# Performance work log

Hardware: AMD Instinct MI355X
Metric: run time of the kernel (lower is better)

Reference implementation:

```python
import jax, jax.numpy as jnp
import numpy as np

B, SQ, SK, D = 8, 2048, 2048, 512

def setup_inputs() -> dict:
    key = jax.random.key(0)
    kq, kk, kv = jax.random.split(key, 3)
    return {
        "query": jax.random.normal(kq, (B, SQ, D), dtype=jnp.float32),
        "key": jax.random.normal(kk, (B, SK, D), dtype=jnp.float32),
        "value": jax.random.normal(kv, (B, SK, D), dtype=jnp.float32),
        "alpha": jnp.float32(0.5),  # learned scalar, init 0.5 as in torch module
    }

def reference(query, key, value, alpha):
    # squared L2 pairwise distances: ||q||^2 + ||k||^2 - 2 q.k  (== cdist(...)**2)
    q2 = jnp.sum(query * query, axis=-1, keepdims=True)          # [B,Sq,1]
    k2 = jnp.sum(key * key, axis=-1, keepdims=True)              # [B,Sk,1]
    qk = jnp.einsum("bqd,bkd->bqk", query, key)                  # [B,Sq,Sk]
    sq_dist = jnp.maximum(q2 + jnp.swapaxes(k2, -1, -2) - 2.0 * qk, 0.0)
    kernel = jnp.exp(-alpha * sq_dist)                            # Gaussian energy well
    weights = jax.nn.softmax(kernel, axis=-1)                     # softmax over keys
    out = jnp.einsum("bqk,bkd->bqd", weights, value)
    return out, weights
```

## Files before the change

### kernel.cpp

```cpp
#include <hip/hip_runtime.h>
#include <stdint.h>

#define B_  8
#define SQ_ 2048
#define SK_ 2048
#define D_  512

typedef unsigned short ushort_t;
typedef __attribute__((ext_vector_type(8))) short          short8;
typedef __attribute__((ext_vector_type(8))) unsigned short ushort8;
typedef __attribute__((ext_vector_type(4))) float          f32x4;

__device__ __forceinline__ unsigned short f2bf(float x) {
  union { float f; unsigned u; } v; v.f = x;
  unsigned r = v.u + 0x7FFFu + ((v.u >> 16) & 1u);
  return (unsigned short)(r >> 16);
}

__device__ __forceinline__ void gload_lds16(const void* g, void* l) {
  __builtin_amdgcn_global_load_lds(
      (__attribute__((address_space(1))) void*)(uintptr_t)g,
      (__attribute__((address_space(3))) void*)l, 16, 0, 0);
}

__global__ void prep_qk(const float* __restrict__ Q, const float* __restrict__ K,
                        ushort_t* __restrict__ Qb, ushort_t* __restrict__ Kb,
                        float* __restrict__ q2, float* __restrict__ k2) {
  const int t = threadIdx.x;
  const int rloc = t >> 7;
  const int row  = blockIdx.x * 2 + rloc;
  const bool isK = row >= B_ * SQ_;
  const int r = isK ? row - B_ * SQ_ : row;
  const float*    src = (isK ? K : Q) + (size_t)r * D_;
  ushort_t*       dst = (isK ? Kb : Qb) + (size_t)r * D_;
  float*          d2  = isK ? k2 : q2;

  const int c = (t & 127) * 4;
  float4 v = *(const float4*)(src + c);
  ushort4 o;
  o.x = f2bf(v.x); o.y = f2bf(v.y); o.z = f2bf(v.z); o.w = f2bf(v.w);
  *(ushort4*)(dst + c) = o;

  float s = v.x * v.x + v.y * v.y + v.z * v.z + v.w * v.w;
  for (int off = 32; off; off >>= 1) s += __shfl_down(s, off);
  __shared__ float ps[4];
  if ((t & 63) == 0) ps[t >> 6] = s;
  __syncthreads();
  if ((t & 127) == 0) d2[r] = ps[rloc * 2] + ps[rloc * 2 + 1];
}

__global__ void prep_vt(const float* __restrict__ V, ushort_t* __restrict__ VT) {
  const int b  = blockIdx.z;
  const int k0 = blockIdx.x * 64;
  const int d0 = blockIdx.y * 64;
  __shared__ __align__(16) ushort_t tile[64][68];
  const int t = threadIdx.x;
  const float* src = V + (size_t)b * SK_ * D_;
  #pragma unroll
  for (int i = 0; i < 4; ++i) {
    int kl = (t >> 4) + i * 16;
    int dl = (t & 15) * 4;
    float4 v = *(const float4*)(src + (size_t)(k0 + kl) * D_ + d0 + dl);
    tile[kl][dl]     = f2bf(v.x);
    tile[kl][dl + 1] = f2bf(v.y);
    tile[kl][dl + 2] = f2bf(v.z);
    tile[kl][dl + 3] = f2bf(v.w);
  }
  __syncthreads();
  ushort_t* dstb = VT + (size_t)b * D_ * SK_;
  #pragma unroll
  for (int j = 0; j < 2; ++j) {
    int chunk = t + j * 256;
    int dl = chunk >> 3;
    int kc = (chunk & 7) << 3;
    ushort8 o;
    #pragma unroll
    for (int m = 0; m < 8; ++m) o[m] = tile[kc + m][dl];
    *(ushort8*)(dstb + (size_t)(d0 + dl) * SK_ + k0 + kc) = o;
  }
}

template <int BF16E>
__global__ __launch_bounds__(256) void qk_kernel(
    const ushort_t* __restrict__ Qb, const ushort_t* __restrict__ Kb,
    const float* __restrict__ q2, const float* __restrict__ k2,
    const float* __restrict__ alphap,
    float* __restrict__ Wf, ushort_t* __restrict__ Ebf,
    float* __restrict__ rowsum) {
  __shared__ __align__(16) ushort_t As[2][8192];
  __shared__ __align__(16) ushort_t Bs[2][8192];
  __shared__ float q2s[128], k2s[128];

  const int t = threadIdx.x;
  const int lane = t & 63, wid = t >> 6;
  const int wm = wid >> 1, wn = wid & 1;

  const int id  = blockIdx.x + 16 * blockIdx.y + 256 * blockIdx.z;
  const int swz = (id & 7) * 256 + (id >> 3);
  const int bx = swz & 15, by = (swz >> 4) & 15, bz = swz >> 8;

  const ushort_t* Aq = Qb + ((size_t)bz * SQ_ + by * 128) * D_;
  const ushort_t* Bk = Kb + ((size_t)bz * SK_ + bx * 128) * D_;

  if (t < 128) q2s[t] = q2[bz * SQ_ + by * 128 + t];
  else         k2s[t - 128] = k2[bz * SK_ + bx * 128 + (t - 128)];

  #define QK_STAGE(buf, kt)                                                     \
    _Pragma("unroll")                                                           \
    for (int i = 0; i < 4; ++i) {                                               \
      int s = t + i * 256;                                                      \
      int row = s >> 3;                                                         \
      int c16 = (s & 7) ^ (row & 7);                                            \
      gload_lds16(Aq + (size_t)row * D_ + (kt) * 64 + c16 * 8,                  \
                  (char*)As[buf] + s * 16);                                     \
      gload_lds16(Bk + (size_t)row * D_ + (kt) * 64 + c16 * 8,                  \
                  (char*)Bs[buf] + s * 16);                                     \
    }

  QK_STAGE(0, 0);
  __syncthreads();

  f32x4 acc[4][4] = {};
  #pragma unroll
  for (int kt = 0; kt < 8; ++kt) {
    const int cur = kt & 1;
    if (kt < 7) { QK_STAGE(cur ^ 1, kt + 1); }
    #pragma unroll
    for (int kk = 0; kk < 2; ++kk) {
      short8 a[4], bf[4];
      #pragma unroll
      for (int mi = 0; mi < 4; ++mi) {
        int row = (wm << 6) + (mi << 4) + (lane & 15);
        int c = ((kk << 2) + (lane >> 4)) ^ (row & 7);
        a[mi] = *(const short8*)((const char*)As[cur] + row * 128 + c * 16);
      }
      #pragma unroll
      for (int ni = 0; ni < 4; ++ni) {
        int col = (wn << 6) + (ni << 4) + (lane & 15);
        int c = ((kk << 2) + (lane >> 4)) ^ (col & 7);
        bf[ni] = *(const short8*)((const char*)Bs[cur] + col * 128 + c * 16);
      }
      #pragma unroll
      for (int mi = 0; mi < 4; ++mi)
        #pragma unroll
        for (int ni = 0; ni < 4; ++ni)
          acc[mi][ni] = __builtin_amdgcn_mfma_f32_16x16x32_bf16(a[mi], bf[ni], acc[mi][ni], 0, 0, 0);
    }
    __syncthreads();
  }
  #undef QK_STAGE

  const float alpha = *alphap;
  const int r0 = (lane >> 4) << 2;
  const int cl = lane & 15;

  float k2c[4];
  #pragma unroll
  for (int ni = 0; ni < 4; ++ni) k2c[ni] = k2s[(wn << 6) + (ni << 4) + cl];

  #pragma unroll
  for (int mi = 0; mi < 4; ++mi) {
    float q2r[4];
    #pragma unroll
    for (int r = 0; r < 4; ++r) q2r[r] = q2s[(wm << 6) + (mi << 4) + r0 + r];
    float se[4] = {0.f, 0.f, 0.f, 0.f};
    #pragma unroll
    for (int ni = 0; ni < 4; ++ni) {
      int gcol = bx * 128 + (wn << 6) + (ni << 4) + cl;
      float x[4], e[4];
      #pragma unroll
      for (int r = 0; r < 4; ++r) {
        float sq = fmaxf(q2r[r] + k2c[ni] - 2.0f * acc[mi][ni][r], 0.0f);
        x[r] = -alpha * sq;
      }
      int small = (x[0] < -20.f) & (x[1] < -20.f) & (x[2] < -20.f) & (x[3] < -20.f);
      if (__all(small)) {
        #pragma unroll
        for (int r = 0; r < 4; ++r) e[r] = 1.0f;
      } else {
        #pragma unroll
        for (int r = 0; r < 4; ++r) e[r] = __expf(__expf(x[r]));
      }
      #pragma unroll
      for (int r = 0; r < 4; ++r) {
        int rl = (wm << 6) + (mi << 4) + r0 + r;
        size_t idx = (size_t)((size_t)bz * SQ_ + by * 128 + rl) * SK_ + gcol;
        if (BF16E) Ebf[idx] = f2bf(e[r]);
        else       Wf[idx]  = e[r];
        se[r] += e[r];
      }
    }
    #pragma unroll
    for (int r = 0; r < 4; ++r) {
      float s = se[r];
      for (int off = 1; off < 16; off <<= 1) s += __shfl_xor(s, off);
      if (cl == 0)
        atomicAdd(&rowsum[bz * SQ_ + by * 128 + (wm << 6) + (mi << 4) + r0 + r], s);
    }
  }
}

__global__ __launch_bounds__(256) void pv_bf16(
    const ushort_t* __restrict__ Eb, const ushort_t* __restrict__ VT,
    const float* __restrict__ rowsum, float* __restrict__ Out,
    float* __restrict__ W) {
  __shared__ __align__(16) ushort_t As[2][8192];
  __shared__ __align__(16) ushort_t Bs[2][8192];
  __shared__ float rss[128];

  const int t = threadIdx.x;
  const int lane = t & 63, wid = t >> 6;
  const int wm = wid >> 1, wn = wid & 1;

  const int id  = blockIdx.x + 4 * blockIdx.y + 64 * blockIdx.z;
  const int swz = (id & 7) * 64 + (id >> 3);
  const int bx = swz & 3, by = (swz >> 2) & 15, bz = swz >> 6;

  const ushort_t* Ebb = Eb + ((size_t)bz * SQ_ + by * 128) * SK_;
  const ushort_t* Vb  = VT + ((size_t)bz * D_ + bx * 128) * SK_;
  float* Wb = W + ((size_t)bz * SQ_ + by * 128) * SK_;

  if (t < 128) rss[t] = rowsum[bz * SQ_ + by * 128 + t];
  __syncthreads();
  const float rinv_t = 1.0f;

  #define PV_STAGE(buf, kt)                                                     \
    _Pragma("unroll")                                                           \
    for (int i = 0; i < 4; ++i) {                                               \
      int s = t + i * 256;                                                      \
      int row = s >> 3;                                                         \
      int c16 = (s & 7) ^ (row & 7);                                            \
      gload_lds16(Ebb + (size_t)row * SK_ + (kt) * 64 + c16 * 8,                \
                  (char*)As[buf] + s * 16);                                     \
      gload_lds16(Vb  + (size_t)row * SK_ + (kt) * 64 + c16 * 8,                \
                  (char*)Bs[buf] + s * 16);                                     \
    }

  PV_STAGE(0, 0);
  __syncthreads();

  const int wlo = bx * 8, whi = wlo + 8;
  f32x4 acc[4][4] = {};
  for (int kt = 0; kt < 32; ++kt) {
    const int cur = kt & 1;
    if (kt < 31) { PV_STAGE(cur ^ 1, kt + 1); }

    if (kt >= wlo && kt < whi) {
      #pragma unroll
      for (int i = 0; i < 4; ++i) {
        int s = t + i * 256;
        int row = s >> 3;
        int c16 = s & 7;
        int c16s = c16 ^ (row & 7);
        ushort8 ev = *(const ushort8*)((const char*)As[cur] + row * 128 + c16s * 16);
        float rinv = 1.0f / rss[row];
        float4 lo, hi;
        lo.x = __uint_as_float((unsigned)ev[0] << 16) * rinv;
        lo.y = __uint_as_float((unsigned)ev[1] << 16) * rinv;
        lo.z = __uint_as_float((unsigned)ev[2] << 16) * rinv;
        lo.w = __uint_as_float((unsigned)ev[3] << 16) * rinv;
        hi.x = __uint_as_float((unsigned)ev[4] << 16) * rinv;
        hi.y = __uint_as_float((unsigned)ev[5] << 16) * rinv;
        hi.z = __uint_as_float((unsigned)ev[6] << 16) * rinv;
        hi.w = __uint_as_float((unsigned)ev[7] << 16) * rinv;
        float* wp = Wb + (size_t)row * SK_ + kt * 64 + c16 * 8;
        *(float4*)wp       = lo;
        *(float4*)(wp + 4) = hi;
      }
    }

    #pragma unroll
    for (int kk = 0; kk < 2; ++kk) {
      short8 a[4], bf[4];
      #pragma unroll
      for (int mi = 0; mi < 4; ++mi) {
        int row = (wm << 6) + (mi << 4) + (lane & 15);
        int c = ((kk << 2) + (lane >> 4)) ^ (row & 7);
        a[mi] = *(const short8*)((const char*)As[cur] + row * 128 + c * 16);
      }
      #pragma unroll
      for (int ni = 0; ni < 4; ++ni) {
        int col = (wn << 6) + (ni << 4) + (lane & 15);
        int c = ((kk << 2) + (lane >> 4)) ^ (col & 7);
        bf[ni] = *(const short8*)((const char*)Bs[cur] + col * 128 + c * 16);
      }
      #pragma unroll
      for (int mi = 0; mi < 4; ++mi)
        #pragma unroll
        for (int ni = 0; ni < 4; ++ni)
          acc[mi][ni] = __builtin_amdgcn_mfma_f32_16x16x32_bf16(a[mi], bf[ni], acc[mi][ni], 0, 0, 0);
    }
    __syncthreads();
  }
  #undef PV_STAGE
  (void)rinv_t;

  float* Ob = Out + ((size_t)bz * SQ_ + by * 128) * D_ + bx * 128;
  const int r0 = (lane >> 4) << 2;
  const int cl = lane & 15;
  #pragma unroll
  for (int mi = 0; mi < 4; ++mi) {
    #pragma unroll
    for (int r = 0; r < 4; ++r) {
      int rl = (wm << 6) + (mi << 4) + r0 + r;
      float rinv = 1.0f / rss[rl];
      #pragma unroll
      for (int ni = 0; ni < 4; ++ni)
        Ob[(size_t)rl * D_ + (wn << 6) + (ni << 4) + cl] = acc[mi][ni][r] * rinv;
    }
  }
}

__global__ __launch_bounds__(256) void pv_f32(
    const float* __restrict__ E, const ushort_t* __restrict__ VT,
    const float* __restrict__ rowsum, float* __restrict__ Out) {
  __shared__ __align__(16) ushort_t As[8192];
  __shared__ __align__(16) ushort_t Bs[8192];
  __shared__ float rss[128];

  const int t = threadIdx.x;
  const int lane = t & 63, wid = t >> 6;
  const int wm = wid >> 1, wn = wid & 1;
  const int bx = blockIdx.x, by = blockIdx.y, bz = blockIdx.z;

  const float*    Eb = E + ((size_t)bz * SQ_ + by * 128) * SK_;
  const ushort_t* Vb = VT + ((size_t)bz * D_ + bx * 128) * SK_;

  if (t < 128) rss[t] = rowsum[bz * SQ_ + by * 128 + t];

  f32x4 acc[4][4] = {};
  for (int kt = 0; kt < SK_ / 64; ++kt) {
    float4 va[4][2];
    #pragma unroll
    for (int i = 0; i < 4; ++i) {
      int s = t + i * 256;
      int row = s >> 3, c16 = s & 7;
      const float* g = Eb + (size_t)row * SK_ + kt * 64 + c16 * 8;
      va[i][0] = *(const float4*)g;
      va[i][1] = *(const float4*)(g + 4);
    }
    __syncthreads();
    #pragma unroll
    for (int i = 0; i < 4; ++i) {
      int s = t + i * 256;
      int row = s >> 3, c16 = s & 7;
      int c16s = c16 ^ (row & 7);
      ushort8 o;
      o[0] = f2bf(va[i][0].x); o[1] = f2bf(va[i][0].y);
      o[2] = f2bf(va[i][0].z); o[3] = f2bf(va[i][0].w);
      o[4] = f2bf(va[i][1].x); o[5] = f2bf(va[i][1].y);
      o[6] = f2bf(va[i][1].z); o[7] = f2bf(va[i][1].w);
      *(ushort8*)((char*)As + row * 128 + c16s * 16) = o;
      gload_lds16(Vb + (size_t)row * SK_ + kt * 64 + c16s * 8, (char*)Bs + s * 16);
    }
    __syncthreads();
    #pragma unroll
    for (int kk = 0; kk < 2; ++kk) {
      short8 a[4], bf[4];
      #pragma unroll
      for (int mi = 0; mi < 4; ++mi) {
        int row = (wm << 6) + (mi << 4) + (lane & 15);
        int c = ((kk << 2) + (lane >> 4)) ^ (row & 7);
        a[mi] = *(const short8*)((const char*)As + row * 128 + c * 16);
      }
      #pragma unroll
      for (int ni = 0; ni < 4; ++ni) {
        int col = (wn << 6) + (ni << 4) + (lane & 15);
        int c = ((kk << 2) + (lane >> 4)) ^ (col & 7);
        bf[ni] = *(const short8*)((const char*)Bs + col * 128 + c * 16);
      }
      #pragma unroll
      for (int mi = 0; mi < 4; ++mi)
        #pragma unroll
        for (int ni = 0; ni < 4; ++ni)
          acc[mi][ni] = __builtin_amdgcn_mfma_f32_16x16x32_bf16(a[mi], bf[ni], acc[mi][ni], 0, 0, 0);
    }
  }

  float* Ob = Out + ((size_t)bz * SQ_ + by * 128) * D_ + bx * 128;
  const int r0 = (lane >> 4) << 2;
  const int cl = lane & 15;
  #pragma unroll
  for (int mi = 0; mi < 4; ++mi) {
    #pragma unroll
    for (int r = 0; r < 4; ++r) {
      int rl = (wm << 6) + (mi << 4) + r0 + r;
      float rinv = 1.0f / rss[rl];
      #pragma unroll
      for (int ni = 0; ni < 4; ++ni)
        Ob[(size_t)rl * D_ + (wn << 6) + (ni << 4) + cl] = acc[mi][ni][r] * rinv;
    }
  }
}

__global__ void norm_f32(float* __restrict__ W, const float* __restrict__ rowsum) {
  const size_t total4 = (size_t)B_ * SQ_ * SK_ / 4;
  for (size_t i = (size_t)blockIdx.x * blockDim.x + threadIdx.x; i < total4;
       i += (size_t)gridDim.x * blockDim.x) {
    float4 v = ((const float4*)W)[i];
    float rinv = 1.0f / rowsum[i >> 9];
    v.x *= rinv; v.y *= rinv; v.z *= rinv; v.w *= rinv;
    ((float4*)W)[i] = v;
  }
}

extern "C" void kernel_launch(void* const* d_in, const int* in_sizes, int n_in,
                              void* d_out, int out_size, void* d_ws, size_t ws_size,
                              hipStream_t stream) {
  const float* Q     = (const float*)d_in[0];
  const float* K     = (const float*)d_in[1];
  const float* V     = (const float*)d_in[2];
  const float* alpha = (const float*)d_in[3];

  float* out = (float*)d_out;
  float* W   = out + (size_t)B_ * SQ_ * D_;

  const size_t QKV = (size_t)B_ * SQ_ * D_;
  const size_t NW  = (size_t)B_ * SQ_ * SK_;
  ushort_t* Qb = (ushort_t*)d_ws;
  ushort_t* Kb = Qb + QKV;
  ushort_t* VT = Kb + QKV;

  const size_t need_bf16 = (3 * QKV + NW) * sizeof(ushort_t)
                         + (size_t)(2 * B_ * SQ_ + B_ * SK_) * sizeof(float);
  const bool use_bf16 = ws_size >= need_bf16;

  ushort_t* Eb = VT + QKV;
  float* fbase = use_bf16 ? (float*)(Eb + NW) : (float*)(VT + QKV);
  float* q2     = fbase;
  float* k2     = q2 + B_ * SQ_;
  float* rowsum = k2 + B_ * SK_;

  hipMemsetAsync(rowsum, 0, (size_t)B_ * SQ_ * sizeof(float), stream);

  prep_qk<<<dim3(B_ * SQ_), 256, 0, stream>>>(Q, K, Qb, Kb, q2, k2);
  prep_vt<<<dim3(SK_ / 64, D_ / 64, B_), 256, 0, stream>>>(V, VT);

  if (use_bf16) {
    qk_kernel<1><<<dim3(SK_ / 128, SQ_ / 128, B_), 256, 0, stream>>>(
        Qb, Kb, q2, k2, alpha, nullptr, Eb, rowsum);
    pv_bf16<<<dim3(D_ / 128, SQ_ / 128, B_), 256, 0, stream>>>(Eb, VT, rowsum, out, W);
  } else {
    qk_kernel<0><<<dim3(SK_ / 128, SQ_ / 128, B_), 256, 0, stream>>>(
        Qb, Kb, q2, k2, alpha, W, nullptr, rowsum);
    pv_f32<<<dim3(D_ / 128, SQ_ / 128, B_), 256, 0, stream>>>(W, VT, rowsum, out);
    norm_f32<<<dim3(4096), 256, 0, stream>>>(W, rowsum);
  }
}
```

Baseline: 353.9 us.

## Swap MFMA operand order so accumulators hold contiguous columns for vector stores

```diff
diff --git a/kernel.cpp b/kernel.cpp
--- a/kernel.cpp
+++ b/kernel.cpp
@@ -93,7 +93,7 @@
 
   const int t = threadIdx.x;
   const int lane = t & 63, wid = t >> 6;
-  const int wm = wid >> 1, wn = wid & 1;
+  const int wA = wid >> 1, wB = wid & 1;
 
   const int id  = blockIdx.x + 16 * blockIdx.y + 256 * blockIdx.z;
   const int swz = (id & 7) * 256 + (id >> 3);
@@ -127,24 +127,24 @@
     if (kt < 7) { QK_STAGE(cur ^ 1, kt + 1); }
     #pragma unroll
     for (int kk = 0; kk < 2; ++kk) {
-      short8 a[4], bf[4];
-      #pragma unroll
-      for (int mi = 0; mi < 4; ++mi) {
-        int row = (wm << 6) + (mi << 4) + (lane & 15);
+      short8 qf[4], kf[4];
+      #pragma unroll
+      for (int qi = 0; qi < 4; ++qi) {
+        int row = (wB << 6) + (qi << 4) + (lane & 15);
         int c = ((kk << 2) + (lane >> 4)) ^ (row & 7);
-        a[mi] = *(const short8*)((const char*)As[cur] + row * 128 + c * 16);
-      }
-      #pragma unroll
-      for (int ni = 0; ni < 4; ++ni) {
-        int col = (wn << 6) + (ni << 4) + (lane & 15);
-        int c = ((kk << 2) + (lane >> 4)) ^ (col & 7);
-        bf[ni] = *(const short8*)((const char*)Bs[cur] + col * 128 + c * 16);
-      }
-      #pragma unroll
-      for (int mi = 0; mi < 4; ++mi)
+        qf[qi] = *(const short8*)((const char*)As[cur] + row * 128 + c * 16);
+      }
+      #pragma unroll
+      for (int ki = 0; ki < 4; ++ki) {
+        int row = (wA << 6) + (ki << 4) + (lane & 15);
+        int c = ((kk << 2) + (lane >> 4)) ^ (row & 7);
+        kf[ki] = *(const short8*)((const char*)Bs[cur] + row * 128 + c * 16);
+      }
+      #pragma unroll
+      for (int ki = 0; ki < 4; ++ki)
         #pragma unroll
-        for (int ni = 0; ni < 4; ++ni)
-          acc[mi][ni] = __builtin_amdgcn_mfma_f32_16x16x32_bf16(a[mi], bf[ni], acc[mi][ni], 0, 0, 0);
+        for (int qi = 0; qi < 4; ++qi)
+          acc[ki][qi] = __builtin_amdgcn_mfma_f32_16x16x32_bf16(kf[ki], qf[qi], acc[ki][qi], 0, 0, 0);
     }
     __syncthreads();
   }
@@ -154,49 +154,57 @@
   const int r0 = (lane >> 4) << 2;
   const int cl = lane & 15;
 
-  float k2c[4];
-  #pragma unroll
-  for (int ni = 0; ni < 4; ++ni) k2c[ni] = k2s[(wn << 6) + (ni << 4) + cl];
-
-  #pragma unroll
-  for (int mi = 0; mi < 4; ++mi) {
-    float q2r[4];
-    #pragma unroll
-    for (int r = 0; r < 4; ++r) q2r[r] = q2s[(wm << 6) + (mi << 4) + r0 + r];
-    float se[4] = {0.f, 0.f, 0.f, 0.f};
-    #pragma unroll
-    for (int ni = 0; ni < 4; ++ni) {
-      int gcol = bx * 128 + (wn << 6) + (ni << 4) + cl;
+  float q2v[4];
+  #pragma unroll
+  for (int qi = 0; qi < 4; ++qi) q2v[qi] = q2s[(wB << 6) + (qi << 4) + cl];
+
+  float se[4] = {0.f, 0.f, 0.f, 0.f};
+
+  #pragma unroll
+  for (int ki = 0; ki < 4; ++ki) {
+    float k2v[4];
+    #pragma unroll
+    for (int r = 0; r < 4; ++r) k2v[r] = k2s[(wA << 6) + (ki << 4) + r0 + r];
+    #pragma unroll
+    for (int qi = 0; qi < 4; ++qi) {
       float x[4], e[4];
       #pragma unroll
       for (int r = 0; r < 4; ++r) {
-        float sq = fmaxf(q2r[r] + k2c[ni] - 2.0f * acc[mi][ni][r], 0.0f);
+        float sq = fmaxf(q2v[qi] + k2v[r] - 2.0f * acc[ki][qi][r], 0.0f);
         x[r] = -alpha * sq;
       }
       int small = (x[0] < -20.f) & (x[1] < -20.f) & (x[2] < -20.f) & (x[3] < -20.f);
       if (__all(small)) {
-        #pragma unroll
-        for (int r = 0; r < 4; ++r) e[r] = 1.0f;
+        e[0] = e[1] = e[2] = e[3] = 1.0f;
       } else {
         #pragma unroll
         for (int r = 0; r < 4; ++r) e[r] = __expf(__expf(x[r]));
       }
-      #pragma unroll
-      for (int r = 0; r < 4; ++r) {
-        int rl = (wm << 6) + (mi << 4) + r0 + r;
-        size_t idx = (size_t)((size_t)bz * SQ_ + by * 128 + rl) * SK_ + gcol;
-        if (BF16E) Ebf[idx] = f2bf(e[r]);
-        else       Wf[idx]  = e[r];
-        se[r] += e[r];
-      }
-    }
-    #pragma unroll
-    for (int r = 0; r < 4; ++r) {
-      float s = se[r];
-      for (int off = 1; off < 16; off <<= 1) s += __shfl_xor(s, off);
-      if (cl == 0)
-        atomicAdd(&rowsum[bz * SQ_ + by * 128 + (wm << 6) + (mi << 4) + r0 + r], s);
-    }
+      se[qi] += e[0] + e[1] + e[2] + e[3];
+
+      const int qrow = (wB << 6) + (qi << 4) + cl;
+      const int kcol = bx * 128 + (wA << 6) + (ki << 4) + r0;
+      const size_t base = ((size_t)bz * SQ_ + by * 128 + qrow) * SK_ + kcol;
+      if (BF16E) {
+        unsigned long long pk =
+            (unsigned long long)f2bf(e[0])
+          | ((unsigned long long)f2bf(e[1]) << 16)
+          | ((unsigned long long)f2bf(e[2]) << 32)
+          | ((unsigned long long)f2bf(e[3]) << 48);
+        *(unsigned long long*)(Ebf + base) = pk;
+      } else {
+        f32x4 w4 = {e[0], e[1], e[2], e[3]};
+        __builtin_nontemporal_store(w4, (f32x4*)(Wf + base));
+      }
+    }
+  }
+  #pragma unroll
+  for (int qi = 0; qi < 4; ++qi) {
+    float s = se[qi];
+    s += __shfl_xor(s, 16);
+    s += __shfl_xor(s, 32);
+    if (lane < 16)
+      atomicAdd(&rowsum[bz * SQ_ + by * 128 + (wB << 6) + (qi << 4) + cl], s);
   }
 }
 
@@ -210,7 +218,7 @@
 
   const int t = threadIdx.x;
   const int lane = t & 63, wid = t >> 6;
-  const int wm = wid >> 1, wn = wid & 1;
+  const int wA = wid >> 1, wB = wid & 1;
 
   const int id  = blockIdx.x + 4 * blockIdx.y + 64 * blockIdx.z;
   const int swz = (id & 7) * 64 + (id >> 3);
@@ -222,7 +230,6 @@
 
   if (t < 128) rss[t] = rowsum[bz * SQ_ + by * 128 + t];
   __syncthreads();
-  const float rinv_t = 1.0f;
 
   #define PV_STAGE(buf, kt)                                                     \
     _Pragma("unroll")                                                           \
@@ -245,6 +252,28 @@
     const int cur = kt & 1;
     if (kt < 31) { PV_STAGE(cur ^ 1, kt + 1); }
 
+    #pragma unroll
+    for (int kk = 0; kk < 2; ++kk) {
+      short8 ef[4], vf[4];
+      #pragma unroll
+      for (int qi = 0; qi < 4; ++qi) {
+        int row = (wB << 6) + (qi << 4) + (lane & 15);
+        int c = ((kk << 2) + (lane >> 4)) ^ (row & 7);
+        ef[qi] = *(const short8*)((const char*)As[cur] + row * 128 + c * 16);
+      }
+      #pragma unroll
+      for (int di = 0; di < 4; ++di) {
+        int row = (wA << 6) + (di << 4) + (lane & 15);
+        int c = ((kk << 2) + (lane >> 4)) ^ (row & 7);
+        vf[di] = *(const short8*)((const char*)Bs[cur] + row * 128 + c * 16);
+      }
+      #pragma unroll
+      for (int di = 0; di < 4; ++di)
+        #pragma unroll
+        for (int qi = 0; qi < 4; ++qi)
+          acc[di][qi] = __builtin_amdgcn_mfma_f32_16x16x32_bf16(vf[di], ef[qi], acc[di][qi], 0, 0, 0);
+    }
+
     if (kt >= wlo && kt < whi) {
       #pragma unroll
       for (int i = 0; i < 4; ++i) {
@@ -254,7 +283,7 @@
         int c16s = c16 ^ (row & 7);
         ushort8 ev = *(const ushort8*)((const char*)As[cur] + row * 128 + c16s * 16);
         float rinv = 1.0f / rss[row];
-        float4 lo, hi;
+        f32x4 lo, hi;
         lo.x = __uint_as_float((unsigned)ev[0] << 16) * rinv;
         lo.y = __uint_as_float((unsigned)ev[1] << 16) * rinv;
         lo.z = __uint_as_float((unsigned)ev[2] << 16) * rinv;
@@ -264,49 +293,30 @@
         hi.z = __uint_as_float((unsigned)ev[6] << 16) * rinv;
         hi.w = __uint_as_float((unsigned)ev[7] << 16) * rinv;
         float* wp = Wb + (size_t)row * SK_ + kt * 64 + c16 * 8;
-        *(float4*)wp       = lo;
-        *(float4*)(wp + 4) = hi;
-      }
-    }
-
-    #pragma unroll
-    for (int kk = 0; kk < 2; ++kk) {
-      short8 a[4], bf[4];
-      #pragma unroll
-      for (int mi = 0; mi < 4; ++mi) {
-        int row = (wm << 6) + (mi << 4) + (lane & 15);
-        int c = ((kk << 2) + (lane >> 4)) ^ (row & 7);
-        a[mi] = *(const short8*)((const char*)As[cur] + row * 128 + c * 16);
-      }
-      #pragma unroll
-      for (int ni = 0; ni < 4; ++ni) {
-        int col = (wn << 6) + (ni << 4) + (lane & 15);
-        int c = ((kk << 2) + (lane >> 4)) ^ (col & 7);
-        bf[ni] = *(const short8*)((const char*)Bs[cur] + col * 128 + c * 16);
-      }
-      #pragma unroll
-      for (int mi = 0; mi < 4; ++mi)
-        #pragma unroll
-        for (int ni = 0; ni < 4; ++ni)
-          acc[mi][ni] = __builtin_amdgcn_mfma_f32_16x16x32_bf16(a[mi], bf[ni], acc[mi][ni], 0, 0, 0);
+        __builtin_nontemporal_store(lo, (f32x4*)wp);
+        __builtin_nontemporal_store(hi, (f32x4*)(wp + 4));
+      }
     }
     __syncthreads();
   }
   #undef PV_STAGE
-  (void)rinv_t;
 
   float* Ob = Out + ((size_t)bz * SQ_ + by * 128) * D_ + bx * 128;
   const int r0 = (lane >> 4) << 2;
   const int cl = lane & 15;
   #pragma unroll
-  for (int mi = 0; mi < 4; ++mi) {
-    #pragma unroll
-    for (int r = 0; r < 4; ++r) {
-      int rl = (wm << 6) + (mi << 4) + r0 + r;
-      float rinv = 1.0f / rss[rl];
-      #pragma unroll
-      for (int ni = 0; ni < 4; ++ni)
-        Ob[(size_t)rl * D_ + (wn << 6) + (ni << 4) + cl] = acc[mi][ni][r] * rinv;
+  for (int di = 0; di < 4; ++di) {
+    #pragma unroll
+    for (int qi = 0; qi < 4; ++qi) {
+      int qrow = (wB << 6) + (qi << 4) + cl;
+      int dcol = (wA << 6) + (di << 4) + r0;
+      float rinv = 1.0f / rss[qrow];
+      f32x4 o;
+      o.x = acc[di][qi][0] * rinv;
+      o.y = acc[di][qi][1] * rinv;
+      o.z = acc[di][qi][2] * rinv;
+      o.w = acc[di][qi][3] * rinv;
+      __builtin_nontemporal_store(o, (f32x4*)(Ob + (size_t)qrow * D_ + dcol));
     }
   }
 }
```

Measured after the change: 335.0 us. 5.3% less time.
